# Optimization experiments

Hardware: AMD Instinct MI355X
Metric: run time of the kernel (lower is better)

The kernel has to match this reference:

```python
import jax, jax.numpy as jnp
import numpy as np

N_HEAD, D_K = 8, 16

def _ln(x, g, b):
    m = jnp.mean(x, -1, keepdims=True)
    v = jnp.var(x, -1, keepdims=True)
    return (x - m) * jax.lax.rsqrt(v + 1e-5) * g + b

def _enc_layer(x, wq, bq, wk, bk, wv, bv, wo, bo, g1, be1, cw1, cb1, cw2, cb2, g2, be2):
    B, L, D = x.shape
    q = (x @ wq + bq).reshape(B, L, N_HEAD, D_K)
    k = (x @ wk + bk).reshape(B, L, N_HEAD, D_K)
    v = (x @ wv + bv).reshape(B, L, N_HEAD, D_K)
    attn = jnp.einsum('blhd,bmhd->bhlm', q, k) / jnp.sqrt(jnp.float32(D_K))
    attn = jax.nn.softmax(attn, axis=-1)
    o = jnp.einsum('bhlm,bmhd->blhd', attn, v).reshape(B, L, -1)
    x = _ln(o @ wo + bo + x, g1, be1)          # post-LN residual (MHA)
    h = jax.nn.relu(x @ cw1 + cb1)             # 1x1 conv == linear
    return _ln(h @ cw2 + cb2 + x, g2, be2)     # post-LN residual (FFN)

def setup_inputs() -> dict:
    key = jax.random.key(0)
    ks = jax.random.split(key, 20)
    N, D, NNZ = 100000, 128, 2000000
    B, L, NL, DI = 32, 256, 2, 512
    s = 0.02
    inp = {}
    inp['ego'] = jax.random.normal(ks[0], (N, D), jnp.float32)
    inp['vals'] = jax.random.uniform(ks[1], (NNZ,), jnp.float32) / 20.0  # ~normalized adj values
    inp['W1'] = jax.random.normal(ks[2], (D, D), jnp.float32) * s
    inp['b1'] = jnp.zeros((D,), jnp.float32)
    inp['W2'] = jax.random.normal(ks[3], (D, D), jnp.float32) * s
    inp['b2'] = jnp.zeros((D,), jnp.float32)
    inp['enc_in'] = jax.random.normal(ks[4], (B, L, D), jnp.float32)
    inp['wq'] = jax.random.normal(ks[5], (NL, D, D), jnp.float32) * s
    inp['bq'] = jnp.zeros((NL, D), jnp.float32)
    inp['wk'] = jax.random.normal(ks[6], (NL, D, D), jnp.float32) * s
    inp['bk'] = jnp.zeros((NL, D), jnp.float32)
    inp['wv'] = jax.random.normal(ks[7], (NL, D, D), jnp.float32) * s
    inp['bv'] = jnp.zeros((NL, D), jnp.float32)
    inp['wo'] = jax.random.normal(ks[8], (NL, D, D), jnp.float32) * s
    inp['bo'] = jnp.zeros((NL, D), jnp.float32)
    inp['ln1_g'] = jnp.ones((NL, D), jnp.float32)
    inp['ln1_b'] = jnp.zeros((NL, D), jnp.float32)
    inp['cw1'] = jax.random.normal(ks[9], (NL, D, DI), jnp.float32) * s
    inp['cb1'] = jnp.zeros((NL, DI), jnp.float32)
    inp['cw2'] = jax.random.normal(ks[10], (NL, DI, D), jnp.float32) * s
    inp['cb2'] = jnp.zeros((NL, D), jnp.float32)
    inp['ln2_g'] = jnp.ones((NL, D), jnp.float32)
    inp['ln2_b'] = jnp.zeros((NL, D), jnp.float32)
    inp['rows'] = jnp.sort(jax.random.randint(ks[11], (NNZ,), 0, N, jnp.int32))
    inp['cols'] = jax.random.randint(ks[12], (NNZ,), 0, N, jnp.int32)
    return inp

def reference(ego, vals, W1, b1, W2, b2, enc_in, wq, bq, wk, bk, wv, bv, wo, bo,
              ln1_g, ln1_b, cw1, cb1, cw2, cb2, ln2_g, ln2_b, rows, cols):
    N = ego.shape[0]
    # sparse A_in @ ego  (COO SpMM via gather + segment_sum)
    side = jax.ops.segment_sum(vals[:, None] * ego[cols], rows, num_segments=N)
    # bi-interaction aggregator (dropout=identity in eval)
    sum_emb = jax.nn.leaky_relu((ego + side) @ W1 + b1)
    bi_emb = jax.nn.leaky_relu((ego * side) @ W2 + b2)
    agg = sum_emb + bi_emb
    # transformer encoder over edge sequences
    x = enc_in
    for i in range(wq.shape[0]):
        x = _enc_layer(x, wq[i], bq[i], wk[i], bk[i], wv[i], bv[i], wo[i], bo[i],
                       ln1_g[i], ln1_b[i], cw1[i], cb1[i], cw2[i], cb2[i], ln2_g[i], ln2_b[i])
    return (agg, x)
```

## Files before the change

### kernel.cpp

```cpp
#include <hip/hip_runtime.h>

typedef __attribute__((ext_vector_type(8))) short bf16x8;
typedef __attribute__((ext_vector_type(4))) float f32x4;

__device__ __forceinline__ unsigned short f2b(float f) {
    union { float f; unsigned int i; } u; u.f = f;
    return (unsigned short)((u.i + 0x7FFFu + ((u.i >> 16) & 1u)) >> 16);
}
__device__ __forceinline__ unsigned int packbf2(float a, float b) {
    return (unsigned int)f2b(a) | ((unsigned int)f2b(b) << 16);
}

__global__ __launch_bounds__(256) void ego2bf16_kernel(
    const float* __restrict__ ego, unsigned int* __restrict__ egob, size_t n4)
{
    size_t i = (size_t)blockIdx.x * 256 + threadIdx.x;
    size_t stride = (size_t)gridDim.x * 256;
    for (; i < n4; i += stride) {
        float4 a = *(const float4*)(ego + i * 4);
        uint2 p;
        p.x = packbf2(a.x, a.y);
        p.y = packbf2(a.z, a.w);
        *(uint2*)(egob + i * 2) = p;
    }
}

__device__ __forceinline__ void spmm_block(
    const unsigned int* __restrict__ egob, const float* __restrict__ vals,
    const int* __restrict__ rows, const int* __restrict__ cols,
    float* __restrict__ side, int nnz, int blk)
{
    int tid = threadIdx.x;
    int wave = tid >> 6, lane = tid & 63;
    int e0 = blk * 256 + wave * 64;
    if (e0 >= nnz) return;

    int idx = e0 + lane;
    int last = nnz - 1;
    bool ok = idx < nnz;
    int safe = ok ? idx : last;
    int my_row = rows[safe];
    int my_col = cols[safe];
    float my_val = ok ? vals[safe] : 0.f;

    unsigned int pre[16];
    #pragma unroll
    for (int j = 0; j < 16; ++j) {
        unsigned int c = (unsigned int)__builtin_amdgcn_readlane(my_col, j);
        pre[j] = *(egob + ((size_t)c << 6) + lane);
    }

    float ax = 0.f, ay = 0.f;
    int cur = __builtin_amdgcn_readlane(my_row, 0);
    #pragma unroll
    for (int e = 0; e < 64; ++e) {
        int r = __builtin_amdgcn_readlane(my_row, e);
        float vv = __int_as_float(__builtin_amdgcn_readlane(__float_as_int(my_val), e));
        unsigned int u = pre[e & 15];
        if (e < 48) {
            unsigned int c = (unsigned int)__builtin_amdgcn_readlane(my_col, e + 16);
            pre[e & 15] = *(egob + ((size_t)c << 6) + lane);
        }
        if (r != cur) {
            atomicAdd(&side[(size_t)cur * 128 + lane * 2], ax);
            atomicAdd(&side[(size_t)cur * 128 + lane * 2 + 1], ay);
            ax = 0.f; ay = 0.f; cur = r;
        }
        ax = fmaf(vv, __uint_as_float(u << 16), ax);
        ay = fmaf(vv, __uint_as_float(u & 0xFFFF0000u), ay);
    }
    atomicAdd(&side[(size_t)cur * 128 + lane * 2], ax);
    atomicAdd(&side[(size_t)cur * 128 + lane * 2 + 1], ay);
}

#define LDAB 40

__device__ __forceinline__ void gemm2_core(
    const float* __restrict__ A, const float* __restrict__ W,
    const float* __restrict__ bias, const float* __restrict__ R,
    const float* __restrict__ g, const float* __restrict__ bta,
    float* __restrict__ C, int M, int N, int K, int act,
    int bm, int bn, unsigned short* As, unsigned short* Bs,
    float* redS, float* redSS)
{
    int tid = threadIdx.x, wave = tid >> 6, lane = tid & 63;
    int lm = lane & 15, quad = lane >> 4;
    int wm = wave >> 1, wn = wave & 1;

    f32x4 acc[2][4];
    #pragma unroll
    for (int i = 0; i < 2; ++i)
        #pragma unroll
        for (int j = 0; j < 4; ++j) acc[i][j] = (f32x4)(0.f);

    for (int k0 = 0; k0 < K; k0 += 32) {
        {
            int m = tid >> 2, kc = (tid & 3) * 8;
            const float* p = A + (size_t)(bm + m) * K + k0 + kc;
            float4 a0 = *(const float4*)p, a1 = *(const float4*)(p + 4);
            uint4 pk;
            pk.x = packbf2(a0.x, a0.y); pk.y = packbf2(a0.z, a0.w);
            pk.z = packbf2(a1.x, a1.y); pk.w = packbf2(a1.z, a1.w);
            *(uint4*)&As[m * LDAB + kc] = pk;
        }
        {
            int nn = tid & 127, kh = (tid >> 7) * 16;
            const float* p = W + (size_t)(k0 + kh) * N + bn + nn;
            float w[16];
            #pragma unroll
            for (int j = 0; j < 16; ++j) w[j] = p[(size_t)j * N];
            uint4 pk;
            pk.x = packbf2(w[0], w[1]);  pk.y = packbf2(w[2], w[3]);
            pk.z = packbf2(w[4], w[5]);  pk.w = packbf2(w[6], w[7]);
            *(uint4*)&Bs[nn * LDAB + kh] = pk;
            pk.x = packbf2(w[8], w[9]);  pk.y = packbf2(w[10], w[11]);
            pk.z = packbf2(w[12], w[13]); pk.w = packbf2(w[14], w[15]);
            *(uint4*)&Bs[nn * LDAB + kh + 8] = pk;
        }
        __syncthreads();
        bf16x8 af[2], bfr[4];
        #pragma unroll
        for (int mi = 0; mi < 2; ++mi)
            af[mi] = *(bf16x8*)&As[(wm * 32 + mi * 16 + lm) * LDAB + quad * 8];
        #pragma unroll
        for (int ni = 0; ni < 4; ++ni)
            bfr[ni] = *(bf16x8*)&Bs[(wn * 64 + ni * 16 + lm) * LDAB + quad * 8];
        #pragma unroll
        for (int mi = 0; mi < 2; ++mi)
            #pragma unroll
            for (int ni = 0; ni < 4; ++ni)
                acc[mi][ni] = __builtin_amdgcn_mfma_f32_16x16x32_bf16(
                    af[mi], bfr[ni], acc[mi][ni], 0, 0, 0);
        __syncthreads();
    }

    #pragma unroll
    for (int mi = 0; mi < 2; ++mi) {
        #pragma unroll
        for (int r = 0; r < 4; ++r) {
            int row = bm + wm * 32 + mi * 16 + quad * 4 + r;
            #pragma unroll
            for (int ni = 0; ni < 4; ++ni) {
                int col = bn + wn * 64 + ni * 16 + lm;
                float v = acc[mi][ni][r] + bias[col];
                if (R) v += R[(size_t)row * N + col];
                if (act) v = fmaxf(v, 0.f);
                acc[mi][ni][r] = v;
            }
        }
    }

    if (g) {
        #pragma unroll
        for (int mi = 0; mi < 2; ++mi) {
            #pragma unroll
            for (int r = 0; r < 4; ++r) {
                float s = 0.f, ss = 0.f;
                #pragma unroll
                for (int ni = 0; ni < 4; ++ni) {
                    float v = acc[mi][ni][r];
                    s += v; ss = fmaf(v, v, ss);
                }
                #pragma unroll
                for (int off = 1; off < 16; off <<= 1) {
                    s  += __shfl_xor(s, off, 64);
                    ss += __shfl_xor(ss, off, 64);
                }
                if (lm == 0) {
                    int lr = wm * 32 + mi * 16 + quad * 4 + r;
                    redS[wn * 64 + lr] = s;
                    redSS[wn * 64 + lr] = ss;
                }
            }
        }
        __syncthreads();
        #pragma unroll
        for (int mi = 0; mi < 2; ++mi) {
            #pragma unroll
            for (int r = 0; r < 4; ++r) {
                int lr = wm * 32 + mi * 16 + quad * 4 + r;
                int row = bm + lr;
                float s = redS[lr] + redS[64 + lr];
                float ss = redSS[lr] + redSS[64 + lr];
                float mean = s * (1.f / 128.f);
                float var = ss * (1.f / 128.f) - mean * mean;
                float rstd = rsqrtf(var + 1e-5f);
                #pragma unroll
                for (int ni = 0; ni < 4; ++ni) {
                    int col = wn * 64 + ni * 16 + lm;
                    float y = (acc[mi][ni][r] - mean) * rstd * g[col] + bta[col];
                    C[(size_t)row * 128 + col] = y;
                }
            }
        }
    } else {
        #pragma unroll
        for (int mi = 0; mi < 2; ++mi) {
            #pragma unroll
            for (int r = 0; r < 4; ++r) {
                int row = bm + wm * 32 + mi * 16 + quad * 4 + r;
                #pragma unroll
                for (int ni = 0; ni < 4; ++ni) {
                    int col = bn + wn * 64 + ni * 16 + lm;
                    C[(size_t)row * N + col] = acc[mi][ni][r];
                }
            }
        }
    }
}

__device__ __forceinline__ void bi_core(
    const float* __restrict__ ego, const float* __restrict__ side,
    const float* __restrict__ W1, const float* __restrict__ b1,
    const float* __restrict__ W2, const float* __restrict__ b2,
    float* __restrict__ out, int M, int bm, int bn,
    unsigned short* Us, unsigned short* Ms,
    unsigned short* W1s, unsigned short* W2s)
{
    int tid = threadIdx.x, wave = tid >> 6, lane = tid & 63;
    int lm = lane & 15, quad = lane >> 4;

    f32x4 acc1[2][4], acc2[2][4];
    #pragma unroll
    for (int i = 0; i < 2; ++i)
        #pragma unroll
        for (int j = 0; j < 4; ++j) { acc1[i][j] = (f32x4)(0.f); acc2[i][j] = (f32x4)(0.f); }

    for (int k0 = 0; k0 < 128; k0 += 32) {
        #pragma unroll
        for (int it = 0; it < 2; ++it) {
            int i = tid + it * 256;
            int m = i >> 2, kc = (i & 3) * 8;
            int gm = bm + m;
            float e[8], s[8];
            if (gm < M) {
                const float* pe = ego + (size_t)gm * 128 + k0 + kc;
                const float* ps = side + (size_t)gm * 128 + k0 + kc;
                float4 e0 = *(const float4*)pe, e1 = *(const float4*)(pe + 4);
                float4 s0 = *(const float4*)ps, s1 = *(const float4*)(ps + 4);
                e[0]=e0.x; e[1]=e0.y; e[2]=e0.z; e[3]=e0.w;
                e[4]=e1.x; e[5]=e1.y; e[6]=e1.z; e[7]=e1.w;
                s[0]=s0.x; s[1]=s0.y; s[2]=s0.z; s[3]=s0.w;
                s[4]=s1.x; s[5]=s1.y; s[6]=s1.z; s[7]=s1.w;
            } else {
                #pragma unroll
                for (int j = 0; j < 8; ++j) { e[j] = 0.f; s[j] = 0.f; }
            }
            uint4 pu, pm;
            pu.x = packbf2(e[0]+s[0], e[1]+s[1]); pu.y = packbf2(e[2]+s[2], e[3]+s[3]);
            pu.z = packbf2(e[4]+s[4], e[5]+s[5]); pu.w = packbf2(e[6]+s[6], e[7]+s[7]);
            pm.x = packbf2(e[0]*s[0], e[1]*s[1]); pm.y = packbf2(e[2]*s[2], e[3]*s[3]);
            pm.z = packbf2(e[4]*s[4], e[5]*s[5]); pm.w = packbf2(e[6]*s[6], e[7]*s[7]);
            *(uint4*)&Us[m * LDAB + kc] = pu;
            *(uint4*)&Ms[m * LDAB + kc] = pm;
        }
        {
            int nn = tid & 63, kq = (tid >> 6) * 8;
            const float* p1 = W1 + (size_t)(k0 + kq) * 128 + bn + nn;
            const float* p2 = W2 + (size_t)(k0 + kq) * 128 + bn + nn;
            float wa[8], wb[8];
            #pragma unroll
            for (int j = 0; j < 8; ++j) { wa[j] = p1[(size_t)j * 128]; wb[j] = p2[(size_t)j * 128]; }
            uint4 pk1, pk2;
            pk1.x = packbf2(wa[0],wa[1]); pk1.y = packbf2(wa[2],wa[3]);
            pk1.z = packbf2(wa[4],wa[5]); pk1.w = packbf2(wa[6],wa[7]);
            pk2.x = packbf2(wb[0],wb[1]); pk2.y = packbf2(wb[2],wb[3]);
            pk2.z = packbf2(wb[4],wb[5]); pk2.w = packbf2(wb[6],wb[7]);
            *(uint4*)&W1s[nn * LDAB + kq] = pk1;
            *(uint4*)&W2s[nn * LDAB + kq] = pk2;
        }
        __syncthreads();
        bf16x8 au[2], am[2], bf1[4], bf2[4];
        #pragma unroll
        for (int mi = 0; mi < 2; ++mi) {
            au[mi] = *(bf16x8*)&Us[(wave * 32 + mi * 16 + lm) * LDAB + quad * 8];
            am[mi] = *(bf16x8*)&Ms[(wave * 32 + mi * 16 + lm) * LDAB + quad * 8];
        }
        #pragma unroll
        for (int ni = 0; ni < 4; ++ni) {
            bf1[ni] = *(bf16x8*)&W1s[(ni * 16 + lm) * LDAB + quad * 8];
            bf2[ni] = *(bf16x8*)&W2s[(ni * 16 + lm) * LDAB + quad * 8];
        }
        #pragma unroll
        for (int mi = 0; mi < 2; ++mi)
            #pragma unroll
            for (int ni = 0; ni < 4; ++ni) {
                acc1[mi][ni] = __builtin_amdgcn_mfma_f32_16x16x32_bf16(
                    au[mi], bf1[ni], acc1[mi][ni], 0, 0, 0);
                acc2[mi][ni] = __builtin_amdgcn_mfma_f32_16x16x32_bf16(
                    am[mi], bf2[ni], acc2[mi][ni], 0, 0, 0);
            }
        __syncthreads();
    }
    #pragma unroll
    for (int mi = 0; mi < 2; ++mi) {
        #pragma unroll
        for (int r = 0; r < 4; ++r) {
            int row = bm + wave * 32 + mi * 16 + quad * 4 + r;
            if (row < M) {
                #pragma unroll
                for (int ni = 0; ni < 4; ++ni) {
                    int col = bn + ni * 16 + lm;
                    float v1 = acc1[mi][ni][r] + b1[col];
                    v1 = v1 > 0.f ? v1 : 0.01f * v1;
                    float v2 = acc2[mi][ni][r] + b2[col];
                    v2 = v2 > 0.f ? v2 : 0.01f * v2;
                    out[(size_t)row * 128 + col] = v1 + v2;
                }
            }
        }
    }
}


__global__ __launch_bounds__(256) void qkv2_spmm(
    const float* __restrict__ A,
    const float* __restrict__ wq, const float* __restrict__ wk, const float* __restrict__ wv,
    const float* __restrict__ bq, const float* __restrict__ bk, const float* __restrict__ bv,
    float* __restrict__ Q, float* __restrict__ Ko, float* __restrict__ V, int M, int encGy,
    const unsigned int* __restrict__ egob, const float* __restrict__ vals,
    const int* __restrict__ rows, const int* __restrict__ cols,
    float* __restrict__ side, int nnz, int spmmBase, int encN)
{
    __shared__ unsigned short As[64 * LDAB];
    __shared__ unsigned short Bs[128 * LDAB];
    __shared__ float redS[128], redSS[128];
    int gid = blockIdx.x;
    if (gid >= encN) {
        spmm_block(egob, vals, rows, cols, side, nnz, spmmBase + gid - encN);
        return;
    }
    int sel = gid / encGy, by = gid % encGy;
    const float* W = (sel == 0) ? wq : (sel == 1) ? wk : wv;
    const float* b = (sel == 0) ? bq : (sel == 1) ? bk : bv;
    float* C = (sel == 0) ? Q : (sel == 1) ? Ko : V;
    gemm2_core(A, W, b, nullptr, nullptr, nullptr, C, M, 128, 128, 0,
               by * 64, 0, As, Bs, redS, redSS);
}

__global__ __launch_bounds__(256) void gemm2_spmm(
    const float* __restrict__ A, const float* __restrict__ W,
    const float* __restrict__ bias, const float* __restrict__ R,
    const float* __restrict__ g, const float* __restrict__ bta,
    float* __restrict__ C, int M, int N, int K, int act, int encGy,
    const unsigned int* __restrict__ egob, const float* __restrict__ vals,
    const int* __restrict__ rows, const int* __restrict__ cols,
    float* __restrict__ side, int nnz, int spmmBase, int encN)
{
    __shared__ unsigned short As[64 * LDAB];
    __shared__ unsigned short Bs[128 * LDAB];
    __shared__ float redS[128], redSS[128];
    int gid = blockIdx.x;
    if (gid >= encN) {
        spmm_block(egob, vals, rows, cols, side, nnz, spmmBase + gid - encN);
        return;
    }
    int bx = gid / encGy, by = gid % encGy;
    gemm2_core(A, W, bias, R, g, bta, C, M, N, K, act,
               by * 64, bx * 128, As, Bs, redS, redSS);
}

__global__ __launch_bounds__(256) void gemm2_bi(
    const float* __restrict__ A, const float* __restrict__ W,
    const float* __restrict__ bias, const float* __restrict__ R,
    const float* __restrict__ g, const float* __restrict__ bta,
    float* __restrict__ C, int M, int N, int K, int act, int encGy, int encN,
    const float* __restrict__ ego, const float* __restrict__ side,
    const float* __restrict__ W1, const float* __restrict__ b1,
    const float* __restrict__ W2, const float* __restrict__ b2,
    float* __restrict__ out, int Mbi, int biBase)
{
    __shared__ char smem[30720];
    int gid = blockIdx.x;
    if (gid < encN) {
        unsigned short* As = (unsigned short*)smem;
        unsigned short* Bs = (unsigned short*)(smem + 5120);
        float* redS  = (float*)(smem + 15360);
        float* redSS = (float*)(smem + 15360 + 512);
        int bx = gid / encGy, by = gid % encGy;
        gemm2_core(A, W, bias, R, g, bta, C, M, N, K, act,
                   by * 64, bx * 128, As, Bs, redS, redSS);
    } else {
        int bb = biBase + (gid - encN);
        unsigned short* Us  = (unsigned short*)smem;
        unsigned short* Ms  = Us + 128 * LDAB;
        unsigned short* W1s = Ms + 128 * LDAB;
        unsigned short* W2s = W1s + 64 * LDAB;
        bi_core(ego, side, W1, b1, W2, b2, out, Mbi,
                (bb >> 1) * 128, (bb & 1) * 64, Us, Ms, W1s, W2s);
    }
}

__global__ __launch_bounds__(256) void attn_spmm(
    const float* __restrict__ q, const float* __restrict__ k,
    const float* __restrict__ v, float* __restrict__ o, int NH,
    const unsigned int* __restrict__ egob, const float* __restrict__ vals,
    const int* __restrict__ rows, const int* __restrict__ cols,
    float* __restrict__ side, int nnz, int spmmBase, int encN)
{
    const int L = 256, DK = 16;
    __shared__ float Ks[128 * DK];
    __shared__ float Vs[128 * DK];
    int gid = blockIdx.x;
    if (gid >= encN) {
        spmm_block(egob, vals, rows, cols, side, nnz, spmmBase + gid - encN);
        return;
    }
    int b = gid / NH, h = gid % NH;
    int tid = threadIdx.x;

    size_t qbase = ((size_t)(b * L + tid) * NH + h) * DK;
    float qr[16];
    #pragma unroll
    for (int d4 = 0; d4 < 4; ++d4) {
        float4 t = *(const float4*)(q + qbase + d4 * 4);
        qr[d4*4+0] = t.x * 0.25f; qr[d4*4+1] = t.y * 0.25f;
        qr[d4*4+2] = t.z * 0.25f; qr[d4*4+3] = t.w * 0.25f;
    }
    float acc[16];
    #pragma unroll
    for (int d = 0; d < 16; ++d) acc[d] = 0.f;
    float mmax = -1e30f, ssum = 0.f;

    for (int c0 = 0; c0 < L; c0 += 128) {
        __syncthreads();
        for (int i = tid; i < 128 * 4; i += 256) {
            int ll = i >> 2, d4 = (i & 3) * 4;
            size_t gg = ((size_t)(b * L + c0 + ll) * NH + h) * DK + d4;
            *(float4*)&Ks[ll * 16 + d4] = *(const float4*)(k + gg);
            *(float4*)&Vs[ll * 16 + d4] = *(const float4*)(v + gg);
        }
        __syncthreads();

        for (int kk = 0; kk < 128; ++kk) {
            float dot = 0.f;
            #pragma unroll
            for (int d4 = 0; d4 < 4; ++d4) {
                float4 kv = *(const float4*)&Ks[kk * 16 + d4 * 4];
                dot = fmaf(qr[d4*4+0], kv.x, dot);
                dot = fmaf(qr[d4*4+1], kv.y, dot);
                dot = fmaf(qr[d4*4+2], kv.z, dot);
                dot = fmaf(qr[d4*4+3], kv.w, dot);
            }
            if (dot > mmax) {
                float alpha = __expf(mmax - dot);
                ssum *= alpha;
                #pragma unroll
                for (int d = 0; d < 16; ++d) acc[d] *= alpha;
                mmax = dot;
            }
            float p = __expf(dot - mmax);
            ssum += p;
            #pragma unroll
            for (int d4 = 0; d4 < 4; ++d4) {
                float4 vv = *(const float4*)&Vs[kk * 16 + d4 * 4];
                acc[d4*4+0] = fmaf(p, vv.x, acc[d4*4+0]);
                acc[d4*4+1] = fmaf(p, vv.y, acc[d4*4+1]);
                acc[d4*4+2] = fmaf(p, vv.z, acc[d4*4+2]);
                acc[d4*4+3] = fmaf(p, vv.w, acc[d4*4+3]);
            }
        }
    }
    float inv = 1.f / ssum;
    #pragma unroll
    for (int d4 = 0; d4 < 4; ++d4) {
        float4 t;
        t.x = acc[d4*4+0] * inv; t.y = acc[d4*4+1] * inv;
        t.z = acc[d4*4+2] * inv; t.w = acc[d4*4+3] * inv;
        *(float4*)(o + qbase + d4 * 4) = t;
    }
}

extern "C" void kernel_launch(void* const* d_in, const int* in_sizes, int n_in,
                              void* d_out, int out_size, void* d_ws, size_t ws_size,
                              hipStream_t stream) {
    const float* ego    = (const float*)d_in[0];
    const float* vals   = (const float*)d_in[1];
    const float* W1     = (const float*)d_in[2];
    const float* b1     = (const float*)d_in[3];
    const float* W2     = (const float*)d_in[4];
    const float* b2     = (const float*)d_in[5];
    const float* enc_in = (const float*)d_in[6];
    const float* wq  = (const float*)d_in[7];
    const float* bq  = (const float*)d_in[8];
    const float* wk  = (const float*)d_in[9];
    const float* bk  = (const float*)d_in[10];
    const float* wv  = (const float*)d_in[11];
    const float* bv  = (const float*)d_in[12];
    const float* wo  = (const float*)d_in[13];
    const float* bo  = (const float*)d_in[14];
    const float* ln1_g = (const float*)d_in[15];
    const float* ln1_b = (const float*)d_in[16];
    const float* cw1 = (const float*)d_in[17];
    const float* cb1 = (const float*)d_in[18];
    const float* cw2 = (const float*)d_in[19];
    const float* cb2 = (const float*)d_in[20];
    const float* ln2_g = (const float*)d_in[21];
    const float* ln2_b = (const float*)d_in[22];
    const int* rows = (const int*)d_in[23];
    const int* cols = (const int*)d_in[24];

    const int D = 128, DI = 512, NH = 8, L = 256;
    const int Nn   = in_sizes[0] / D;
    const int nnz  = in_sizes[1];
    const int NL   = in_sizes[7] / (D * D);
    const int Menc = in_sizes[6] / D;
    const int Bb   = Menc / L;

    float* ws = (float*)d_ws;
    size_t off = 0;
    float* side = ws + off; off += (size_t)Nn * D;
    float* Qb = ws + off; off += (size_t)Menc * D;
    float* Kb = ws + off; off += (size_t)Menc * D;
    float* Vb = ws + off; off += (size_t)Menc * D;
    float* Ob = ws + off; off += (size_t)Menc * D;
    float* XA = ws + off; off += (size_t)Menc * D;
    float* XB = ws + off; off += (size_t)Menc * D;
    float* Hb = ws + off; off += (size_t)Menc * DI;
    unsigned int* egob = (unsigned int*)(ws + off); off += (size_t)Nn * (D / 2);

    float* outAgg = (float*)d_out;
    float* outX   = (float*)d_out + (size_t)Nn * D;

    hipMemsetAsync(side, 0, (size_t)Nn * D * sizeof(float), stream);
    ego2bf16_kernel<<<2048, 256, 0, stream>>>(ego, egob, (size_t)Nn * (D / 4));

    const int spmmBlocks = (nnz + 255) / 256;
    const int nStages = 5 * NL - 2;
    const int per = (spmmBlocks + nStages - 1) / nStages;
    const int encGy = Menc / 64;
    const int biGy = (Nn + 127) / 128;
    int ci = 0;

    const float* x = enc_in;
    for (int i = 0; i < NL; ++i) {
        const size_t wOff = (size_t)i * D * D;
        int base, cnt;
        #define NEXT_CHUNK  base = ci * per; cnt = spmmBlocks - base; \
                            if (cnt < 0) cnt = 0; if (cnt > per) cnt = per; ci++

        NEXT_CHUNK;
        qkv2_spmm<<<3 * encGy + cnt, 256, 0, stream>>>(
            x, wq + wOff, wk + wOff, wv + wOff,
            bq + (size_t)i * D, bk + (size_t)i * D, bv + (size_t)i * D,
            Qb, Kb, Vb, Menc, encGy,
            egob, vals, rows, cols, side, nnz, base, 3 * encGy);

        NEXT_CHUNK;
        attn_spmm<<<Bb * NH + cnt, 256, 0, stream>>>(
            Qb, Kb, Vb, Ob, NH,
            egob, vals, rows, cols, side, nnz, base, Bb * NH);

        NEXT_CHUNK;
        gemm2_spmm<<<encGy + cnt, 256, 0, stream>>>(
            Ob, wo + wOff, bo + (size_t)i * D, x,
            ln1_g + (size_t)i * D, ln1_b + (size_t)i * D, XA, Menc, D, D, 0, encGy,
            egob, vals, rows, cols, side, nnz, base, encGy);

        if (i < NL - 1) {
            NEXT_CHUNK;
            gemm2_spmm<<<4 * encGy + cnt, 256, 0, stream>>>(
                XA, cw1 + (size_t)i * D * DI, cb1 + (size_t)i * DI, nullptr,
                nullptr, nullptr, Hb, Menc, DI, D, 1, encGy,
                egob, vals, rows, cols, side, nnz, base, 4 * encGy);
        } else {
            gemm2_bi<<<4 * encGy + biGy, 256, 0, stream>>>(
                XA, cw1 + (size_t)i * D * DI, cb1 + (size_t)i * DI, nullptr,
                nullptr, nullptr, Hb, Menc, DI, D, 1, encGy, 4 * encGy,
                ego, side, W1, b1, W2, b2, outAgg, Nn, 0);
        }

        float* dst = (i == NL - 1) ? outX : XB;
        if (i < NL - 1) {
            NEXT_CHUNK;
            gemm2_spmm<<<encGy + cnt, 256, 0, stream>>>(
                Hb, cw2 + (size_t)i * DI * D, cb2 + (size_t)i * D, XA,
                ln2_g + (size_t)i * D, ln2_b + (size_t)i * D, dst, Menc, D, DI, 0, encGy,
                egob, vals, rows, cols, side, nnz, base, encGy);
        } else {
            gemm2_bi<<<encGy + biGy, 256, 0, stream>>>(
                Hb, cw2 + (size_t)i * DI * D, cb2 + (size_t)i * D, XA,
                ln2_g + (size_t)i * D, ln2_b + (size_t)i * D, dst, Menc, D, DI, 0, encGy, encGy,
                ego, side, W1, b1, W2, b2, outAgg, Nn, biGy);
        }
        #undef NEXT_CHUNK
        x = XB;
    }
}
```

Before: 485.0 us.

## Fold side zeroing and bf16 conversion into first QKV launch, spread bi-aggregation across stages

Removes the standalone memset and ego-to-bf16 kernel by appending zero-fill and conversion blocks to the first QKV GEMM launch. The SpMM work is redistributed over the remaining stages, and the bi-interaction aggregation is retiled to 64-row full-width blocks and split across the last four encoder launches, including the attention kernel, instead of two. This aims to cut launch count and serial tail time by overlapping independent work with the encoder kernels. It adds more shared-memory pressure in the mixed kernels and relies on every SpMM chunk finishing before the bi-aggregation stages that read side.

Result: slower. 502.2 us (+3.5%).

```diff
diff --git a/kernel.cpp b/kernel.cpp
--- a/kernel.cpp
+++ b/kernel.cpp
@@ -9,20 +9,6 @@
 }
 __device__ __forceinline__ unsigned int packbf2(float a, float b) {
     return (unsigned int)f2b(a) | ((unsigned int)f2b(b) << 16);
-}
-
-__global__ __launch_bounds__(256) void ego2bf16_kernel(
-    const float* __restrict__ ego, unsigned int* __restrict__ egob, size_t n4)
-{
-    size_t i = (size_t)blockIdx.x * 256 + threadIdx.x;
-    size_t stride = (size_t)gridDim.x * 256;
-    for (; i < n4; i += stride) {
-        float4 a = *(const float4*)(ego + i * 4);
-        uint2 p;
-        p.x = packbf2(a.x, a.y);
-        p.y = packbf2(a.z, a.w);
-        *(uint2*)(egob + i * 2) = p;
-    }
 }
 
 __device__ __forceinline__ void spmm_block(
@@ -209,16 +195,17 @@
     }
 }
 
-__device__ __forceinline__ void bi_core(
+__device__ __forceinline__ void bi_core2(
     const float* __restrict__ ego, const float* __restrict__ side,
     const float* __restrict__ W1, const float* __restrict__ b1,
     const float* __restrict__ W2, const float* __restrict__ b2,
-    float* __restrict__ out, int M, int bm, int bn,
+    float* __restrict__ out, int M, int bm,
     unsigned short* Us, unsigned short* Ms,
     unsigned short* W1s, unsigned short* W2s)
 {
     int tid = threadIdx.x, wave = tid >> 6, lane = tid & 63;
     int lm = lane & 15, quad = lane >> 4;
+    int wm = wave >> 1, wn = wave & 1;
 
     f32x4 acc1[2][4], acc2[2][4];
     #pragma unroll
@@ -227,10 +214,8 @@
         for (int j = 0; j < 4; ++j) { acc1[i][j] = (f32x4)(0.f); acc2[i][j] = (f32x4)(0.f); }
 
     for (int k0 = 0; k0 < 128; k0 += 32) {
-        #pragma unroll
-        for (int it = 0; it < 2; ++it) {
-            int i = tid + it * 256;
-            int m = i >> 2, kc = (i & 3) * 8;
+        {
+            int m = tid >> 2, kc = (tid & 3) * 8;
             int gm = bm + m;
             float e[8], s[8];
             if (gm < M) {
@@ -255,31 +240,37 @@
             *(uint4*)&Ms[m * LDAB + kc] = pm;
         }
         {
-            int nn = tid & 63, kq = (tid >> 6) * 8;
-            const float* p1 = W1 + (size_t)(k0 + kq) * 128 + bn + nn;
-            const float* p2 = W2 + (size_t)(k0 + kq) * 128 + bn + nn;
-            float wa[8], wb[8];
-            #pragma unroll
-            for (int j = 0; j < 8; ++j) { wa[j] = p1[(size_t)j * 128]; wb[j] = p2[(size_t)j * 128]; }
-            uint4 pk1, pk2;
-            pk1.x = packbf2(wa[0],wa[1]); pk1.y = packbf2(wa[2],wa[3]);
-            pk1.z = packbf2(wa[4],wa[5]); pk1.w = packbf2(wa[6],wa[7]);
-            pk2.x = packbf2(wb[0],wb[1]); pk2.y = packbf2(wb[2],wb[3]);
-            pk2.z = packbf2(wb[4],wb[5]); pk2.w = packbf2(wb[6],wb[7]);
-            *(uint4*)&W1s[nn * LDAB + kq] = pk1;
-            *(uint4*)&W2s[nn * LDAB + kq] = pk2;
+            int nn = tid & 127, kh = (tid >> 7) * 16;
+            const float* p1 = W1 + (size_t)(k0 + kh) * 128 + nn;
+            const float* p2 = W2 + (size_t)(k0 + kh) * 128 + nn;
+            float wa[16], wb[16];
+            #pragma unroll
+            for (int j = 0; j < 16; ++j) { wa[j] = p1[(size_t)j * 128]; wb[j] = p2[(size_t)j * 128]; }
+            uint4 pk;
+            pk.x = packbf2(wa[0], wa[1]);  pk.y = packbf2(wa[2], wa[3]);
+            pk.z = packbf2(wa[4], wa[5]);  pk.w = packbf2(wa[6], wa[7]);
+            *(uint4*)&W1s[nn * LDAB + kh] = pk;
+            pk.x = packbf2(wa[8], wa[9]);  pk.y = packbf2(wa[10], wa[11]);
+            pk.z = packbf2(wa[12], wa[13]); pk.w = packbf2(wa[14], wa[15]);
+            *(uint4*)&W1s[nn * LDAB + kh + 8] = pk;
+            pk.x = packbf2(wb[0], wb[1]);  pk.y = packbf2(wb[2], wb[3]);
+            pk.z = packbf2(wb[4], wb[5]);  pk.w = packbf2(wb[6], wb[7]);
+            *(uint4*)&W2s[nn * LDAB + kh] = pk;
+            pk.x = packbf2(wb[8], wb[9]);  pk.y = packbf2(wb[10], wb[11]);
+            pk.z = packbf2(wb[12], wb[13]); pk.w = packbf2(wb[14], wb[15]);
+            *(uint4*)&W2s[nn * LDAB + kh + 8] = pk;
         }
         __syncthreads();
         bf16x8 au[2], am[2], bf1[4], bf2[4];
         #pragma unroll
         for (int mi = 0; mi < 2; ++mi) {
-            au[mi] = *(bf16x8*)&Us[(wave * 32 + mi * 16 + lm) * LDAB + quad * 8];
-            am[mi] = *(bf16x8*)&Ms[(wave * 32 + mi * 16 + lm) * LDAB + quad * 8];
+            au[mi] = *(bf16x8*)&Us[(wm * 32 + mi * 16 + lm) * LDAB + quad * 8];
+            am[mi] = *(bf16x8*)&Ms[(wm * 32 + mi * 16 + lm) * LDAB + quad * 8];
         }
         #pragma unroll
         for (int ni = 0; ni < 4; ++ni) {
-            bf1[ni] = *(bf16x8*)&W1s[(ni * 16 + lm) * LDAB + quad * 8];
-            bf2[ni] = *(bf16x8*)&W2s[(ni * 16 + lm) * LDAB + quad * 8];
+            bf1[ni] = *(bf16x8*)&W1s[(wn * 64 + ni * 16 + lm) * LDAB + quad * 8];
+            bf2[ni] = *(bf16x8*)&W2s[(wn * 64 + ni * 16 + lm) * LDAB + quad * 8];
         }
         #pragma unroll
         for (int mi = 0; mi < 2; ++mi)
@@ -296,11 +287,11 @@
     for (int mi = 0; mi < 2; ++mi) {
         #pragma unroll
         for (int r = 0; r < 4; ++r) {
-            int row = bm + wave * 32 + mi * 16 + quad * 4 + r;
+            int row = bm + wm * 32 + mi * 16 + quad * 4 + r;
             if (row < M) {
                 #pragma unroll
                 for (int ni = 0; ni < 4; ++ni) {
-                    int col = bn + ni * 16 + lm;
+                    int col = wn * 64 + ni * 16 + lm;
                     float v1 = acc1[mi][ni][r] + b1[col];
                     v1 = v1 > 0.f ? v1 : 0.01f * v1;
                     float v2 = acc2[mi][ni][r] + b2[col];
@@ -312,6 +303,48 @@
     }
 }
 
+
+__global__ __launch_bounds__(256) void qkv2_pre(
+    const float* __restrict__ A,
+    const float* __restrict__ wq, const float* __restrict__ wk, const float* __restrict__ wv,
+    const float* __restrict__ bq, const float* __restrict__ bk, const float* __restrict__ bv,
+    float* __restrict__ Q, float* __restrict__ Ko, float* __restrict__ V, int M, int encGy,
+    float* __restrict__ side, int Nn,
+    const float* __restrict__ ego, unsigned int* __restrict__ egob,
+    int encN, int ZB, int CB)
+{
+    __shared__ unsigned short As[64 * LDAB];
+    __shared__ unsigned short Bs[128 * LDAB];
+    __shared__ float redS[128], redSS[128];
+    int gid = blockIdx.x;
+    int tid = threadIdx.x;
+    if (gid >= encN) {
+        int j = gid - encN;
+        if (j < ZB) {
+            size_t n4 = (size_t)Nn * 32;
+            float4 z = make_float4(0.f, 0.f, 0.f, 0.f);
+            for (size_t i = (size_t)j * 256 + tid; i < n4; i += (size_t)ZB * 256)
+                ((float4*)side)[i] = z;
+        } else {
+            int c = j - ZB;
+            size_t n4 = (size_t)Nn * 32;
+            for (size_t i = (size_t)c * 256 + tid; i < n4; i += (size_t)CB * 256) {
+                float4 a = *(const float4*)(ego + i * 4);
+                uint2 p;
+                p.x = packbf2(a.x, a.y);
+                p.y = packbf2(a.z, a.w);
+                *(uint2*)(egob + i * 2) = p;
+            }
+        }
+        return;
+    }
+    int sel = gid / encGy, by = gid % encGy;
+    const float* W = (sel == 0) ? wq : (sel == 1) ? wk : wv;
+    const float* b = (sel == 0) ? bq : (sel == 1) ? bk : bv;
+    float* C = (sel == 0) ? Q : (sel == 1) ? Ko : V;
+    gemm2_core(A, W, b, nullptr, nullptr, nullptr, C, M, 128, 128, 0,
+               by * 64, 0, As, Bs, redS, redSS);
+}
 
 __global__ __launch_bounds__(256) void qkv2_spmm(
     const float* __restrict__ A,
@@ -360,7 +393,7 @@
                by * 64, bx * 128, As, Bs, redS, redSS);
 }
 
-__global__ __launch_bounds__(256) void gemm2_bi(
+__global__ __launch_bounds__(256) void gemm2_bi2(
     const float* __restrict__ A, const float* __restrict__ W,
     const float* __restrict__ bias, const float* __restrict__ R,
     const float* __restrict__ g, const float* __restrict__ bta,
@@ -383,30 +416,20 @@
     } else {
         int bb = biBase + (gid - encN);
         unsigned short* Us  = (unsigned short*)smem;
-        unsigned short* Ms  = Us + 128 * LDAB;
-        unsigned short* W1s = Ms + 128 * LDAB;
-        unsigned short* W2s = W1s + 64 * LDAB;
-        bi_core(ego, side, W1, b1, W2, b2, out, Mbi,
-                (bb >> 1) * 128, (bb & 1) * 64, Us, Ms, W1s, W2s);
-    }
-}
-
-__global__ __launch_bounds__(256) void attn_spmm(
+        unsigned short* Ms  = (unsigned short*)(smem + 5120);
+        unsigned short* W1s = (unsigned short*)(smem + 10240);
+        unsigned short* W2s = (unsigned short*)(smem + 20480);
+        bi_core2(ego, side, W1, b1, W2, b2, out, Mbi, bb * 64, Us, Ms, W1s, W2s);
+    }
+}
+
+__device__ __forceinline__ void attn_block(
     const float* __restrict__ q, const float* __restrict__ k,
     const float* __restrict__ v, float* __restrict__ o, int NH,
-    const unsigned int* __restrict__ egob, const float* __restrict__ vals,
-    const int* __restrict__ rows, const int* __restrict__ cols,
-    float* __restrict__ side, int nnz, int spmmBase, int encN)
+    int bh, float* Ks, float* Vs)
 {
     const int L = 256, DK = 16;
-    __shared__ float Ks[128 * DK];
-    __shared__ float Vs[128 * DK];
-    int gid = blockIdx.x;
-    if (gid >= encN) {
-        spmm_block(egob, vals, rows, cols, side, nnz, spmmBase + gid - encN);
-        return;
-    }
-    int b = gid / NH, h = gid % NH;
+    int b = bh / NH, h = bh % NH;
     int tid = threadIdx.x;
 
     size_t qbase = ((size_t)(b * L + tid) * NH + h) * DK;
@@ -468,6 +491,47 @@
         t.x = acc[d4*4+0] * inv; t.y = acc[d4*4+1] * inv;
         t.z = acc[d4*4+2] * inv; t.w = acc[d4*4+3] * inv;
         *(float4*)(o + qbase + d4 * 4) = t;
+    }
+}
+
+__global__ __launch_bounds__(256) void attn_spmm(
+    const float* __restrict__ q, const float* __restrict__ k,
+    const float* __restrict__ v, float* __restrict__ o, int NH,
+    const unsigned int* __restrict__ egob, const float* __restrict__ vals,
+    const int* __restrict__ rows, const int* __restrict__ cols,
+    float* __restrict__ side, int nnz, int spmmBase, int encN)
+{
+    __shared__ float Ks[128 * 16];
+    __shared__ float Vs[128 * 16];
+    int gid = blockIdx.x;
+    if (gid >= encN) {
+        spmm_block(egob, vals, rows, cols, side, nnz, spmmBase + gid - encN);
+        return;
+    }
+    attn_block(q, k, v, o, NH, gid, Ks, Vs);
+}
+
+__global__ __launch_bounds__(256) void attn_bi(
+    const float* __restrict__ q, const float* __restrict__ k,
+    const float* __restrict__ v, float* __restrict__ o, int NH, int encN,
+    const float* __restrict__ ego, const float* __restrict__ side,
+    const float* __restrict__ W1, const float* __restrict__ b1,
+    const float* __restrict__ W2, const float* __restrict__ b2,
+    float* __restrict__ out, int Mbi, int biBase)
+{
+    __shared__ char smem[30720];
+    int gid = blockIdx.x;
+    if (gid < encN) {
+        float* Ks = (float*)smem;
+        float* Vs = (float*)(smem + 8192);
+        attn_block(q, k, v, o, NH, gid, Ks, Vs);
+    } else {
+        int bb = biBase + (gid - encN);
+        unsigned short* Us  = (unsigned short*)smem;
+        unsigned short* Ms  = (unsigned short*)(smem + 5120);
+        unsigned short* W1s = (unsigned short*)(smem + 10240);
+        unsigned short* W2s = (unsigned short*)(smem + 20480);
+        bi_core2(ego, side, W1, b1, W2, b2, out, Mbi, bb * 64, Us, Ms, W1s, W2s);
     }
 }
 
@@ -522,68 +586,103 @@
     float* outAgg = (float*)d_out;
     float* outX   = (float*)d_out + (size_t)Nn * D;
 
-    hipMemsetAsync(side, 0, (size_t)Nn * D * sizeof(float), stream);
-    ego2bf16_kernel<<<2048, 256, 0, stream>>>(ego, egob, (size_t)Nn * (D / 4));
-
     const int spmmBlocks = (nnz + 255) / 256;
-    const int nStages = 5 * NL - 2;
-    const int per = (spmmBlocks + nStages - 1) / nStages;
+    const int nSpmmStages = 5 * NL - 5;
+    const int perS = (spmmBlocks + nSpmmStages - 1) / nSpmmStages;
+    const int biTiles = (Nn + 63) / 64;
+    const int perB = (biTiles + 3) / 4;
+    const int biStart = 5 * NL - 3;
     const int encGy = Menc / 64;
-    const int biGy = (Nn + 127) / 128;
-    int ci = 0;
+    const int ZB = 512, CB = 1024;
+    int sidx = 0, sci = 0, bci = 0;
 
     const float* x = enc_in;
     for (int i = 0; i < NL; ++i) {
         const size_t wOff = (size_t)i * D * D;
         int base, cnt;
-        #define NEXT_CHUNK  base = ci * per; cnt = spmmBlocks - base; \
-                            if (cnt < 0) cnt = 0; if (cnt > per) cnt = per; ci++
-
-        NEXT_CHUNK;
-        qkv2_spmm<<<3 * encGy + cnt, 256, 0, stream>>>(
-            x, wq + wOff, wk + wOff, wv + wOff,
-            bq + (size_t)i * D, bk + (size_t)i * D, bv + (size_t)i * D,
-            Qb, Kb, Vb, Menc, encGy,
-            egob, vals, rows, cols, side, nnz, base, 3 * encGy);
-
-        NEXT_CHUNK;
-        attn_spmm<<<Bb * NH + cnt, 256, 0, stream>>>(
-            Qb, Kb, Vb, Ob, NH,
-            egob, vals, rows, cols, side, nnz, base, Bb * NH);
-
-        NEXT_CHUNK;
-        gemm2_spmm<<<encGy + cnt, 256, 0, stream>>>(
-            Ob, wo + wOff, bo + (size_t)i * D, x,
-            ln1_g + (size_t)i * D, ln1_b + (size_t)i * D, XA, Menc, D, D, 0, encGy,
-            egob, vals, rows, cols, side, nnz, base, encGy);
-
-        if (i < NL - 1) {
-            NEXT_CHUNK;
+        #define SPMM_CHUNK base = sci * perS; cnt = spmmBlocks - base; \
+                           if (cnt < 0) cnt = 0; if (cnt > perS) cnt = perS; sci++
+        #define BI_CHUNK   base = bci * perB; cnt = biTiles - base; \
+                           if (cnt < 0) cnt = 0; if (cnt > perB) cnt = perB; bci++
+
+        sidx++;
+        if (sidx == 1) {
+            qkv2_pre<<<3 * encGy + ZB + CB, 256, 0, stream>>>(
+                x, wq + wOff, wk + wOff, wv + wOff,
+                bq + (size_t)i * D, bk + (size_t)i * D, bv + (size_t)i * D,
+                Qb, Kb, Vb, Menc, encGy,
+                side, Nn, ego, egob, 3 * encGy, ZB, CB);
+        } else {
+            SPMM_CHUNK;
+            qkv2_spmm<<<3 * encGy + cnt, 256, 0, stream>>>(
+                x, wq + wOff, wk + wOff, wv + wOff,
+                bq + (size_t)i * D, bk + (size_t)i * D, bv + (size_t)i * D,
+                Qb, Kb, Vb, Menc, encGy,
+                egob, vals, rows, cols, side, nnz, base, 3 * encGy);
+        }
+
+        sidx++;
+        if (sidx >= biStart) {
+            BI_CHUNK;
+            attn_bi<<<Bb * NH + cnt, 256, 0, stream>>>(
+                Qb, Kb, Vb, Ob, NH, Bb * NH,
+                ego, side, W1, b1, W2, b2, outAgg, Nn, base);
+        } else {
+            SPMM_CHUNK;
+            attn_spmm<<<Bb * NH + cnt, 256, 0, stream>>>(
+                Qb, Kb, Vb, Ob, NH,
+                egob, vals, rows, cols, side, nnz, base, Bb * NH);
+        }
+
+        sidx++;
+        if (sidx >= biStart) {
+            BI_CHUNK;
+            gemm2_bi2<<<encGy + cnt, 256, 0, stream>>>(
+                Ob, wo + wOff, bo + (size_t)i * D, x,
+                ln1_g + (size_t)i * D, ln1_b + (size_t)i * D, XA, Menc, D, D, 0,
+                encGy, encGy,
+                ego, side, W1, b1, W2, b2, outAgg, Nn, base);
+        } else {
+            SPMM_CHUNK;
+            gemm2_spmm<<<encGy + cnt, 256, 0, stream>>>(
+                Ob, wo + wOff, bo + (size_t)i * D, x,
+                ln1_g + (size_t)i * D, ln1_b + (size_t)i * D, XA, Menc, D, D, 0, encGy,
+                egob, vals, rows, cols, side, nnz, base, encGy);
+        }
+
+        sidx++;
+        if (sidx >= biStart) {
+            BI_CHUNK;
+            gemm2_bi2<<<4 * encGy + cnt, 256, 0, stream>>>(
+                XA, cw1 + (size_t)i * D * DI, cb1 + (size_t)i * DI, nullptr,
+                nullptr, nullptr, Hb, Menc, DI, D, 1, encGy, 4 * encGy,
+                ego, side, W1, b1, W2, b2, outAgg, Nn, base);
+        } else {
+            SPMM_CHUNK;
             gemm2_spmm<<<4 * encGy + cnt, 256, 0, stream>>>(
                 XA, cw1 + (size_t)i * D * DI, cb1 + (size_t)i * DI, nullptr,
                 nullptr, nullptr, Hb, Menc, DI, D, 1, encGy,
                 egob, vals, rows, cols, side, nnz, base, 4 * encGy);
+        }
+
+        sidx++;
+        float* dst = (i == NL - 1) ? outX : XB;
+        if (sidx >= biStart) {
+            BI_CHUNK;
+            gemm2_bi2<<<encGy + cnt, 256, 0, stream>>>(
+                Hb, cw2 + (size_t)i * DI * D, cb2 + (size_t)i * D, XA,
+                ln2_g + (size_t)i * D, ln2_b + (size_t)i * D, dst, Menc, D, DI, 0,
+                encGy, encGy,
+                ego, side, W1, b1, W2, b2, outAgg, Nn, base);
         } else {
-            gemm2_bi<<<4 * encGy + biGy, 256, 0, stream>>>(
-                XA, cw1 + (size_t)i * D * DI, cb1 + (size_t)i * DI, nullptr,
-                nullptr, nullptr, Hb, Menc, DI, D, 1, encGy, 4 * encGy,
-                ego, side, W1, b1, W2, b2, outAgg, Nn, 0);
-        }
-
-        float* dst = (i == NL - 1) ? outX : XB;
-        if (i < NL - 1) {
-            NEXT_CHUNK;
+            SPMM_CHUNK;
             gemm2_spmm<<<encGy + cnt, 256, 0, stream>>>(
                 Hb, cw2 + (size_t)i * DI * D, cb2 + (size_t)i * D, XA,
                 ln2_g + (size_t)i * D, ln2_b + (size_t)i * D, dst, Menc, D, DI, 0, encGy,
                 egob, vals, rows, cols, side, nnz, base, encGy);
-        } else {
-            gemm2_bi<<<encGy + biGy, 256, 0, stream>>>(
-                Hb, cw2 + (size_t)i * DI * D, cb2 + (size_t)i * D, XA,
-                ln2_g + (size_t)i * D, ln2_b + (size_t)i * D, dst, Menc, D, DI, 0, encGy, encGy,
-                ego, side, W1, b1, W2, b2, outAgg, Nn, biGy);
-        }
-        #undef NEXT_CHUNK
+        }
+        #undef SPMM_CHUNK
+        #undef BI_CHUNK
         x = XB;
     }
 }
```
